# Optimization experiments

Hardware: AMD Instinct MI355X
Metric: run time of the kernel (lower is better)

Reference implementation:

```python
import jax, jax.numpy as jnp
import numpy as np

N_NODES = 100000


def gcn_conv(x, src, dst, W, b, n_nodes):
    """PyG GCNConv: add self-loops, symmetric degree normalization, X W, scatter-add."""
    # Linear transform first (small out dim -> cheaper messages)
    h = x @ W  # [N, F_out]
    # Add self-loops
    loop = jnp.arange(n_nodes, dtype=src.dtype)
    s = jnp.concatenate([src, loop])
    d = jnp.concatenate([dst, loop])
    # Degree (in-degree over dst, incl. self-loops), deg^{-1/2}
    deg = jax.ops.segment_sum(jnp.ones_like(d, dtype=h.dtype), d, num_segments=n_nodes)
    dinv = jnp.where(deg > 0, jax.lax.rsqrt(deg), 0.0)
    norm = dinv[s] * dinv[d]  # [E+N]
    # Gather-scale-scatter aggregation
    msgs = h[s] * norm[:, None]  # [E+N, F_out]
    out = jax.ops.segment_sum(msgs, d, num_segments=n_nodes)
    return out + b


def setup_inputs() -> dict:
    key = jax.random.key(0)
    ks = jax.random.split(key, 4)
    n, f_in, f_hid, f_out = N_NODES, 512, 16, 7
    n_edges = 3200000
    x = jax.random.normal(ks[0], (n, f_in), dtype=jnp.float32)
    edge_index = jax.random.randint(ks[1], (2, n_edges), 0, n, dtype=jnp.int64)
    W1 = jax.random.normal(ks[2], (f_in, f_hid), dtype=jnp.float32) / np.sqrt(f_in)
    b1 = jnp.zeros((f_hid,), dtype=jnp.float32)
    W2 = jax.random.normal(ks[3], (f_hid, f_out), dtype=jnp.float32) / np.sqrt(f_hid)
    b2 = jnp.zeros((f_out,), dtype=jnp.float32)
    return {"x": x, "edge_index": edge_index, "W1": W1, "b1": b1, "W2": W2, "b2": b2}


def reference(x, edge_index, W1, b1, W2, b2):
    n = x.shape[0]
    src, dst = edge_index[0], edge_index[1]
    h = gcn_conv(x, src, dst, W1, b1, n)
    h = jax.nn.relu(h)
    out = gcn_conv(h, src, dst, W2, b2, n)
    return out
```

## Files before the change

### kernel.cpp

```cpp
#include <hip/hip_runtime.h>

#define F_IN 512
#define F_HID 16
#define F_OUT 7
#define BUCKET 128
#define LB 7
#define CHUNK 4096
#define MAXNB 1024
#define BSTR 8192
#define BSTR2 8704

#define RPB 256
#define KC 32
#define KHALF 256
#define LSTRIDE 33

typedef int   int4v   __attribute__((ext_vector_type(4)));
typedef float float2v __attribute__((ext_vector_type(2)));
typedef float float4v __attribute__((ext_vector_type(4)));
typedef unsigned int uint4v __attribute__((ext_vector_type(4)));

static __device__ __forceinline__ unsigned short f2bf(float f) {
    unsigned int u = __float_as_uint(f);
    u += 0x7FFFu + ((u >> 16) & 1u);
    return (unsigned short)(u >> 16);
}
static __device__ __forceinline__ float bf2f(unsigned short s) {
    return __uint_as_float((unsigned int)s << 16);
}

__global__ void k_init(int* __restrict__ cursor, int NB) {
    int i = blockIdx.x * 256 + threadIdx.x;
    if (i < NB) cursor[i] = i * BSTR;
}

__global__ __launch_bounds__(256) void k_place4(
        const int* __restrict__ src, const int* __restrict__ dst,
        int* __restrict__ cursor, int* __restrict__ bedges, int E, int NB) {
    __shared__ int h[MAXNB];
    __shared__ int s[MAXNB];
    __shared__ int sedge[CHUNK];
    __shared__ unsigned short sbkt[CHUNK];
    int t = threadIdx.x, blk = blockIdx.x;
    for (int i = t; i < MAXNB; i += 256) h[i] = 0;
    __syncthreads();
    int base = blk * CHUNK;
    int4v d4[4], s4[4];
#pragma unroll
    for (int it = 0; it < 4; ++it) {
        int e = base + (it * 256 + t) * 4;
        if (e < E) {
            d4[it] = __builtin_nontemporal_load((const int4v*)(dst + e));
            s4[it] = __builtin_nontemporal_load((const int4v*)(src + e));
        } else {
            int sent = NB << LB;
            d4[it].x = sent; d4[it].y = sent; d4[it].z = sent; d4[it].w = sent;
            s4[it].x = 0;    s4[it].y = 0;    s4[it].z = 0;    s4[it].w = 0;
        }
        atomicAdd(&h[d4[it].x >> LB], 1);
        atomicAdd(&h[d4[it].y >> LB], 1);
        atomicAdd(&h[d4[it].z >> LB], 1);
        atomicAdd(&h[d4[it].w >> LB], 1);
    }
    __syncthreads();
    for (int i = t; i < MAXNB; i += 256) s[i] = h[i];
    __syncthreads();
    for (int off = 1; off < MAXNB; off <<= 1) {
        int v[4];
#pragma unroll
        for (int j = 0; j < 4; ++j) {
            int i = t + j * 256;
            v[j] = s[i] + ((i >= off) ? s[i - off] : 0);
        }
        __syncthreads();
#pragma unroll
        for (int j = 0; j < 4; ++j) s[t + j * 256] = v[j];
        __syncthreads();
    }
    for (int i = t; i < MAXNB; i += 256) {
        int incl = s[i], cnt = h[i];
        int excl = incl - cnt;
        h[i] = excl;
        int db = 0;
        if (i < NB && cnt > 0)
            db = atomicAdd(&cursor[i], cnt) - excl;
        s[i] = db;
    }
    __syncthreads();
#pragma unroll
    for (int it = 0; it < 4; ++it) {
        int d, sv, b, p;
        d = d4[it].x; sv = s4[it].x; b = d >> LB; p = atomicAdd(&h[b], 1);
        sedge[p] = (sv << 8) | (d & (BUCKET - 1)); sbkt[p] = (unsigned short)b;
        d = d4[it].y; sv = s4[it].y; b = d >> LB; p = atomicAdd(&h[b], 1);
        sedge[p] = (sv << 8) | (d & (BUCKET - 1)); sbkt[p] = (unsigned short)b;
        d = d4[it].z; sv = s4[it].z; b = d >> LB; p = atomicAdd(&h[b], 1);
        sedge[p] = (sv << 8) | (d & (BUCKET - 1)); sbkt[p] = (unsigned short)b;
        d = d4[it].w; sv = s4[it].w; b = d >> LB; p = atomicAdd(&h[b], 1);
        sedge[p] = (sv << 8) | (d & (BUCKET - 1)); sbkt[p] = (unsigned short)b;
    }
    __syncthreads();
    for (int j = t; j < CHUNK; j += 256) {
        int b = sbkt[j];
        if (b < NB)
            __builtin_nontemporal_store(sedge[j], bedges + s[b] + j);
    }
}

__global__ __launch_bounds__(256) void k_psort(
        const int* __restrict__ cursor, const int* __restrict__ bedges,
        int* __restrict__ bedges2, float* __restrict__ dinv,
        int* __restrict__ node_off, int* __restrict__ node_nq, int n) {
    __shared__ int cnt[BUCKET];
    __shared__ int sc[BUCKET];
    __shared__ int cur[BUCKET];
    __shared__ int sedge[BSTR2];
    int b = blockIdx.x, t = threadIdx.x;
    int base = b * BSTR;
    int ne = cursor[b] - base;
    if (t < BUCKET) cnt[t] = 0;
    __syncthreads();
    int nq = ne >> 2, tail = ne & 3;
    for (int q = t; q < nq; q += 256) {
        int4v v = *(const int4v*)(bedges + base + (q << 2));
        atomicAdd(&cnt[v.x & 127], 1);
        atomicAdd(&cnt[v.y & 127], 1);
        atomicAdd(&cnt[v.z & 127], 1);
        atomicAdd(&cnt[v.w & 127], 1);
    }
    if (t < tail) atomicAdd(&cnt[bedges[base + (nq << 2) + t] & 127], 1);
    __syncthreads();
    int p = 0;
    if (t < BUCKET) { p = (cnt[t] + 3) & ~3; sc[t] = p; }
    __syncthreads();
    for (int off = 1; off < BUCKET; off <<= 1) {
        int v = 0;
        if (t < BUCKET) { v = sc[t]; if (t >= off) v += sc[t - off]; }
        __syncthreads();
        if (t < BUCKET) sc[t] = v;
        __syncthreads();
    }
    if (t < BUCKET) {
        int w = sc[t] - p;
        cur[t] = w;
        int node = b * BUCKET + t;
        if (node < n) {
            dinv[node] = rsqrtf((float)(cnt[t] + 1));
            node_off[node] = b * BSTR2 + w;
            node_nq[node] = p >> 2;
        }
    }
    __syncthreads();
    for (int q = t; q < nq; q += 256) {
        int4v v = *(const int4v*)(bedges + base + (q << 2));
        int pos;
        pos = atomicAdd(&cur[v.x & 127], 1); sedge[pos] = v.x >> 8;
        pos = atomicAdd(&cur[v.y & 127], 1); sedge[pos] = v.y >> 8;
        pos = atomicAdd(&cur[v.z & 127], 1); sedge[pos] = v.z >> 8;
        pos = atomicAdd(&cur[v.w & 127], 1); sedge[pos] = v.w >> 8;
    }
    if (t < tail) {
        int v = bedges[base + (nq << 2) + t];
        int pos = atomicAdd(&cur[v & 127], 1); sedge[pos] = v >> 8;
    }
    __syncthreads();
    if (t < BUCKET) {
        int endc = cur[t];
        for (int i = endc; i < sc[t]; ++i) sedge[i] = n;
    }
    __syncthreads();
    int total = sc[BUCKET - 1];
    int* dst2 = bedges2 + b * BSTR2;
    for (int j4 = t; j4 < (total >> 2); j4 += 256) {
        int4v v = *(const int4v*)(sedge + (j4 << 2));
        __builtin_nontemporal_store(v, (int4v*)(dst2 + (j4 << 2)));
    }
}

__global__ __launch_bounds__(256) void k_gemm1p(
        const float* __restrict__ x, const float* __restrict__ W,
        float* __restrict__ part, int n) {
    __shared__ float xs[RPB * LSTRIDE];
    int b  = blockIdx.x >> 1;
    int ks = blockIdx.x & 1;
    int r0 = b * RPB;
    int t  = threadIdx.x;
    int r  = r0 + t;
    int kbase = ks * KHALF;

    float2v acc2[F_HID / 2];
#pragma unroll
    for (int c = 0; c < F_HID / 2; ++c) acc2[c] = (float2v){0.0f, 0.0f};

    int lr0 = t >> 3;
    int c4  = t & 7;

    for (int kc = 0; kc < KHALF; kc += KC) {
        __syncthreads();
#pragma unroll
        for (int j = 0; j < 8; ++j) {
            int lr = j * 32 + lr0;
            int gr = r0 + lr;
            float4v v = {0.0f, 0.0f, 0.0f, 0.0f};
            if (gr < n)
                v = *(const float4v*)(x + (size_t)gr * F_IN + kbase + kc + c4 * 4);
            float* d = xs + lr * LSTRIDE + c4 * 4;
            d[0] = v.x; d[1] = v.y; d[2] = v.z; d[3] = v.w;
        }
        __syncthreads();
        if (r < n) {
            const float* xrow = xs + t * LSTRIDE;
            const float2v* Wk2 = (const float2v*)(W + (size_t)(kbase + kc) * F_HID);
#pragma unroll
            for (int k = 0; k < KC; ++k) {
                float xv = xrow[k];
#pragma unroll
                for (int c2 = 0; c2 < F_HID / 2; ++c2)
                    acc2[c2] += xv * Wk2[k * (F_HID / 2) + c2];
            }
        }
    }
    if (r < n) {
        const float* a = (const float*)acc2;
        float4v* o = (float4v*)(part + ((size_t)ks * n + r) * F_HID);
        float4v w0 = {a[0],  a[1],  a[2],  a[3]};
        float4v w1 = {a[4],  a[5],  a[6],  a[7]};
        float4v w2 = {a[8],  a[9],  a[10], a[11]};
        float4v w3 = {a[12], a[13], a[14], a[15]};
        o[0] = w0; o[1] = w1; o[2] = w2; o[3] = w3;
    }
}

__global__ void k_fin1(const float* __restrict__ part, const float* __restrict__ dinv,
                       unsigned short* __restrict__ h1b, unsigned short* __restrict__ h2b,
                       int n) {
    int tg = blockIdx.x * 256 + threadIdx.x;
    int r = tg >> 4, c = tg & 15;
    if (r > n) return;
    if (r == n) {
        h1b[(size_t)r * F_HID + c] = 0;
        if (c < 8) h2b[((size_t)r << 3) + c] = 0;
        return;
    }
    float v = part[(size_t)r * F_HID + c] + part[((size_t)n + r) * F_HID + c];
    h1b[(size_t)r * F_HID + c] = f2bf(dinv[r] * v);
}

__global__ __launch_bounds__(1024) void k_aggF1(
        const int* __restrict__ node_off, const int* __restrict__ node_nq,
        const int* __restrict__ bedges2, const unsigned short* __restrict__ h1b,
        const float* __restrict__ dinv, const float* __restrict__ b1,
        const float* __restrict__ W2, unsigned short* __restrict__ h2b, int n) {
    int tg = blockIdx.x * 1024 + threadIdx.x;
    int node = tg >> 4, c = tg & 15;
    if (node >= n) return;
    int off = node_off[node], nq = node_nq[node];
    float acc = bf2f(h1b[(size_t)node * F_HID + c]);
    for (int q = 0; q < nq; ++q) {
        int4v s = *(const int4v*)(bedges2 + off + (q << 2));
        float v0 = bf2f(h1b[(size_t)s.x * F_HID + c]);
        float v1 = bf2f(h1b[(size_t)s.y * F_HID + c]);
        float v2 = bf2f(h1b[(size_t)s.z * F_HID + c]);
        float v3 = bf2f(h1b[(size_t)s.w * F_HID + c]);
        acc += v0 + v1 + v2 + v3;
    }
    float dv = dinv[node];
    float z = fmaxf(dv * acc + b1[c], 0.0f);
    float h[F_OUT];
#pragma unroll
    for (int o = 0; o < F_OUT; ++o) h[o] = z * W2[c * F_OUT + o];
#pragma unroll
    for (int sft = 8; sft >= 1; sft >>= 1)
#pragma unroll
        for (int o = 0; o < F_OUT; ++o) h[o] += __shfl_xor(h[o], sft, 16);
    if (c < 8) {
        unsigned short w = (c < F_OUT) ? f2bf(dv * h[c]) : (unsigned short)0;
        h2b[((size_t)node << 3) + c] = w;
    }
}

__global__ __launch_bounds__(1024) void k_aggF2(
        const int* __restrict__ node_off, const int* __restrict__ node_nq,
        const int* __restrict__ bedges2, const unsigned short* __restrict__ h2b,
        const float* __restrict__ dinv, const float* __restrict__ b2,
        float* __restrict__ out, int n) {
    int tg = blockIdx.x * 1024 + threadIdx.x;
    int node = tg >> 3, c = tg & 7;
    if (node >= n) return;
    int off = node_off[node], nq = node_nq[node];
    float acc = bf2f(h2b[((size_t)node << 3) + c]);
    for (int q = 0; q < nq; ++q) {
        int4v s = *(const int4v*)(bedges2 + off + (q << 2));
        float v0 = bf2f(h2b[((size_t)s.x << 3) + c]);
        float v1 = bf2f(h2b[((size_t)s.y << 3) + c]);
        float v2 = bf2f(h2b[((size_t)s.z << 3) + c]);
        float v3 = bf2f(h2b[((size_t)s.w << 3) + c]);
        acc += v0 + v1 + v2 + v3;
    }
    if (c < F_OUT)
        out[(size_t)node * F_OUT + c] = dinv[node] * acc + b2[c];
}

extern "C" void kernel_launch(void* const* d_in, const int* in_sizes, int n_in,
                              void* d_out, int out_size, void* d_ws, size_t ws_size,
                              hipStream_t stream) {
    const float* x  = (const float*)d_in[0];
    const int*   ei = (const int*)d_in[1];
    const float* W1 = (const float*)d_in[2];
    const float* b1 = (const float*)d_in[3];
    const float* W2 = (const float*)d_in[4];
    const float* b2 = (const float*)d_in[5];
    float* out = (float*)d_out;

    const int n = in_sizes[0] / F_IN;
    const int E = in_sizes[1] / 2;
    const int* src = ei;
    const int* dst = ei + E;

    const int NB = (n + BUCKET - 1) / BUCKET;
    const int PBLK = (E + CHUNK - 1) / CHUNK;

    size_t Np = ((size_t)n + 3) & ~(size_t)3;
    char* ws = (char*)d_ws;
    int*   cursor       = (int*)ws;             ws += MAXNB * 4;
    float* dinv         = (float*)ws;           ws += Np * 4;
    int*   node_off     = (int*)ws;             ws += Np * 4;
    int*   node_nq      = (int*)ws;             ws += Np * 4;
    int*   bedges       = (int*)ws;             ws += (size_t)NB * BSTR * 4;
    int*   bedges2      = (int*)ws;             ws += (size_t)NB * BSTR2 * 4;
    unsigned short* h1b = (unsigned short*)ws;  ws += (Np + 4) * F_HID * 2;
    unsigned short* h2b = (unsigned short*)ws;  ws += (Np + 4) * 8 * 2;
    float* part         = (float*)bedges;

    k_init   <<<(NB + 255) / 256, 256, 0, stream>>>(cursor, NB);
    k_place4 <<<PBLK, 256, 0, stream>>>(src, dst, cursor, bedges, E, NB);
    k_psort  <<<NB, 256, 0, stream>>>(cursor, bedges, bedges2, dinv, node_off, node_nq, n);
    k_gemm1p <<<((n + RPB - 1) / RPB) * 2, 256, 0, stream>>>(x, W1, part, n);
    k_fin1   <<<((n + 1) * 16 + 255) / 256, 256, 0, stream>>>(part, dinv, h1b, h2b, n);
    k_aggF1  <<<((size_t)n * 16 + 1023) / 1024, 1024, 0, stream>>>(node_off, node_nq, bedges2, h1b, dinv, b1, W2, h2b, n);
    k_aggF2  <<<((size_t)n * 8 + 1023) / 1024, 1024, 0, stream>>>(node_off, node_nq, bedges2, h2b, dinv, b2, out, n);
}
```

Baseline: 461.6 us.

## Restructure first-layer GEMM to stage W in LDS and split K across lanes

The X·W1 kernel used to stage x rows in shared memory, with one thread per row and W read from global memory. It now loads the 256x16 half of W into padded LDS once per block. Each group of 8 lanes reads one x row directly into registers with coalesced float4 loads and accumulates a partial dot product over its K slice. A shuffle-xor reduction then combines the partials, and each lane writes two outputs. This removes the x staging loop and its syncs and puts many more blocks in flight, at the cost of reloading W into LDS in every block and extra shuffle work.

```diff
diff --git a/kernel.cpp b/kernel.cpp
--- a/kernel.cpp
+++ b/kernel.cpp
@@ -10,10 +10,8 @@
 #define BSTR 8192
 #define BSTR2 8704
 
-#define RPB 256
-#define KC 32
 #define KHALF 256
-#define LSTRIDE 33
+#define WSTR 9
 
 typedef int   int4v   __attribute__((ext_vector_type(4)));
 typedef float float2v __attribute__((ext_vector_type(2)));
@@ -177,57 +175,57 @@
     }
 }
 
-__global__ __launch_bounds__(256) void k_gemm1p(
+__global__ __launch_bounds__(256) void k_gemm1w(
         const float* __restrict__ x, const float* __restrict__ W,
         float* __restrict__ part, int n) {
-    __shared__ float xs[RPB * LSTRIDE];
+    __shared__ float2v Ws[256 * WSTR];
     int b  = blockIdx.x >> 1;
     int ks = blockIdx.x & 1;
-    int r0 = b * RPB;
     int t  = threadIdx.x;
-    int r  = r0 + t;
     int kbase = ks * KHALF;
 
-    float2v acc2[F_HID / 2];
-#pragma unroll
-    for (int c = 0; c < F_HID / 2; ++c) acc2[c] = (float2v){0.0f, 0.0f};
-
-    int lr0 = t >> 3;
-    int c4  = t & 7;
-
-    for (int kc = 0; kc < KHALF; kc += KC) {
-        __syncthreads();
-#pragma unroll
-        for (int j = 0; j < 8; ++j) {
-            int lr = j * 32 + lr0;
-            int gr = r0 + lr;
-            float4v v = {0.0f, 0.0f, 0.0f, 0.0f};
-            if (gr < n)
-                v = *(const float4v*)(x + (size_t)gr * F_IN + kbase + kc + c4 * 4);
-            float* d = xs + lr * LSTRIDE + c4 * 4;
-            d[0] = v.x; d[1] = v.y; d[2] = v.z; d[3] = v.w;
-        }
-        __syncthreads();
-        if (r < n) {
-            const float* xrow = xs + t * LSTRIDE;
-            const float2v* Wk2 = (const float2v*)(W + (size_t)(kbase + kc) * F_HID);
-#pragma unroll
-            for (int k = 0; k < KC; ++k) {
-                float xv = xrow[k];
-#pragma unroll
-                for (int c2 = 0; c2 < F_HID / 2; ++c2)
-                    acc2[c2] += xv * Wk2[k * (F_HID / 2) + c2];
+    const float2v* Wg = (const float2v*)(W + (size_t)kbase * F_HID);
+#pragma unroll
+    for (int it = 0; it < 8; ++it) {
+        int m = it * 256 + t;
+        Ws[(m >> 3) * WSTR + (m & 7)] = Wg[m];
+    }
+    __syncthreads();
+
+    int r  = b * 32 + (t >> 3);
+    int kl = t & 7;
+    if (r < n) {
+        const float* xr = x + (size_t)r * F_IN + kbase + kl * 4;
+        float4v v[8];
+#pragma unroll
+        for (int i = 0; i < 8; ++i)
+            v[i] = *(const float4v*)(xr + i * 32);
+
+        float2v acc2[8];
+#pragma unroll
+        for (int c2 = 0; c2 < 8; ++c2) acc2[c2] = (float2v){0.0f, 0.0f};
+
+#pragma unroll
+        for (int i = 0; i < 8; ++i) {
+            int kb = i * 32 + kl * 4;
+#pragma unroll
+            for (int j = 0; j < 4; ++j) {
+                float xv = v[i][j];
+                const float2v* wr = Ws + (kb + j) * WSTR;
+#pragma unroll
+                for (int c2 = 0; c2 < 8; ++c2)
+                    acc2[c2] += xv * wr[c2];
             }
         }
-    }
-    if (r < n) {
-        const float* a = (const float*)acc2;
-        float4v* o = (float4v*)(part + ((size_t)ks * n + r) * F_HID);
-        float4v w0 = {a[0],  a[1],  a[2],  a[3]};
-        float4v w1 = {a[4],  a[5],  a[6],  a[7]};
-        float4v w2 = {a[8],  a[9],  a[10], a[11]};
-        float4v w3 = {a[12], a[13], a[14], a[15]};
-        o[0] = w0; o[1] = w1; o[2] = w2; o[3] = w3;
+#pragma unroll
+        for (int m = 1; m <= 4; m <<= 1) {
+#pragma unroll
+            for (int c2 = 0; c2 < 8; ++c2) {
+                acc2[c2].x += __shfl_xor(acc2[c2].x, m);
+                acc2[c2].y += __shfl_xor(acc2[c2].y, m);
+            }
+        }
+        *(float2v*)(part + ((size_t)ks * n + r) * F_HID + kl * 2) = acc2[kl];
     }
 }
 
@@ -319,6 +317,7 @@
 
     const int NB = (n + BUCKET - 1) / BUCKET;
     const int PBLK = (E + CHUNK - 1) / CHUNK;
+    const int NRB = (n + 31) / 32;
 
     size_t Np = ((size_t)n + 3) & ~(size_t)3;
     char* ws = (char*)d_ws;
@@ -335,7 +334,7 @@
     k_init   <<<(NB + 255) / 256, 256, 0, stream>>>(cursor, NB);
     k_place4 <<<PBLK, 256, 0, stream>>>(src, dst, cursor, bedges, E, NB);
     k_psort  <<<NB, 256, 0, stream>>>(cursor, bedges, bedges2, dinv, node_off, node_nq, n);
-    k_gemm1p <<<((n + RPB - 1) / RPB) * 2, 256, 0, stream>>>(x, W1, part, n);
+    k_gemm1w <<<NRB * 2, 256, 0, stream>>>(x, W1, part, n);
     k_fin1   <<<((n + 1) * 16 + 255) / 256, 256, 0, stream>>>(part, dinv, h1b, h2b, n);
     k_aggF1  <<<((size_t)n * 16 + 1023) / 1024, 1024, 0, stream>>>(node_off, node_nq, bedges2, h1b, dinv, b1, W2, h2b, n);
     k_aggF2  <<<((size_t)n * 8 + 1023) / 1024, 1024, 0, stream>>>(node_off, node_nq, bedges2, h2b, dinv, b2, out, n);
```

Result: faster. 428.0 us (-7.3%).
